# Performance work log

Hardware: AMD Instinct MI355X
Metric: run time of the kernel (lower is better)

The kernel has to match this reference:

```python
import jax, jax.numpy as jnp
import numpy as np

NUM_NODES = 100000
NUM_EDGES = 1600000
NUM_GRAPHS = 64
IN_DIM, HID, NCLS = 64, 128, 10


def setup_inputs() -> dict:
    key = jax.random.key(0)
    ks = jax.random.split(key, 12)
    x = jax.random.normal(ks[0], (NUM_NODES, IN_DIM), dtype=jnp.float32)
    src = jax.random.randint(ks[1], (NUM_EDGES,), 0, NUM_NODES, dtype=jnp.int32)
    dst = jax.random.randint(ks[2], (NUM_EDGES,), 0, NUM_NODES, dtype=jnp.int32)
    batch = jnp.sort(jax.random.randint(ks[3], (NUM_NODES,), 0, NUM_GRAPHS, dtype=jnp.int32))
    def glorot(k, shape):
        lim = (6.0 / (shape[0] + shape[1])) ** 0.5
        return jax.random.uniform(k, shape, jnp.float32, -lim, lim)
    return {
        "x": x, "src": src, "dst": dst, "batch": batch,
        "W1": glorot(ks[4], (IN_DIM, HID)), "b1": jnp.zeros((HID,), jnp.float32),
        "W2": glorot(ks[5], (HID, HID)), "b2": jnp.zeros((HID,), jnp.float32),
        "Wl1": glorot(ks[6], (HID, HID // 2)), "bl1": jnp.zeros((HID // 2,), jnp.float32),
        "Wl2": glorot(ks[7], (HID // 2, NCLS)), "bl2": jnp.zeros((NCLS,), jnp.float32),
    }


def gcn_conv(x, W, b, src, dst):
    # GCNConv: out = D^{-1/2} (A + I) D^{-1/2} (x @ W) + b, deg from A+I
    h = x @ W  # [N, H]
    ones = jnp.ones((src.shape[0],), h.dtype)
    deg = jax.ops.segment_sum(ones, dst, num_segments=NUM_NODES) + 1.0  # +1 self-loop
    dinv = jax.lax.rsqrt(deg)  # [N]
    norm = dinv[src] * dinv[dst]  # [E]
    msg = h[src] * norm[:, None]  # [E, H] gather + scale
    agg = jax.ops.segment_sum(msg, dst, num_segments=NUM_NODES)  # scatter-add
    agg = agg + h * (dinv * dinv)[:, None]  # self-loop message
    return agg + b


def reference(x, src, dst, batch, W1, b1, W2, b2, Wl1, bl1, Wl2, bl2):
    h = jax.nn.relu(gcn_conv(x, W1, b1, src, dst))
    h = jax.nn.relu(gcn_conv(h, W2, b2, src, dst))
    # global mean pool per graph
    sums = jax.ops.segment_sum(h, batch, num_segments=NUM_GRAPHS)  # [G, H]
    cnts = jax.ops.segment_sum(jnp.ones((h.shape[0],), h.dtype), batch, num_segments=NUM_GRAPHS)
    pooled = sums / jnp.maximum(cnts, 1.0)[:, None]
    h = jax.nn.relu(pooled @ Wl1 + bl1)
    return h @ Wl2 + bl2  # [G, num_classes]
```

## Files before the change

kernel.cpp:

```cpp
#include <hip/hip_runtime.h>
#include <hip/hip_bf16.h>

#define NODES_N 100000
#define EDGES_E 1600000
#define GRAPHS_G 64

#define BIN_SHIFT 8
#define BIN_NODES 256
#define NBINS 391
#define NB1 512
#define EPB1 3125

typedef unsigned int uint;
typedef unsigned short ushort;
typedef __attribute__((ext_vector_type(8))) short bf16x8;
typedef __attribute__((ext_vector_type(4))) float f32x4;


__device__ inline uint pack_bf2(float lo, float hi) {
    __hip_bfloat162 h2 = __float22bfloat162_rn(make_float2(lo, hi));
    return *reinterpret_cast<uint*>(&h2);
}

__device__ inline void acc_bf2(uint w, float& a0, float& a1) {
    a0 += __uint_as_float(w << 16);
    a1 += __uint_as_float(w & 0xffff0000u);
}

__device__ inline ushort f2bf(float v) {
    __hip_bfloat16 b = __float2bfloat16(v);
    return *reinterpret_cast<ushort*>(&b);
}


__device__ inline void pack_w_one(const float* W, ushort* Wf, int gid, int KS) {
    int j = gid & 7, l = (gid >> 3) & 63, f = gid >> 9;
    int nt = f / KS, ks = f - nt * KS;
    int k = ks * 32 + ((l >> 4) & 3) * 8 + j;
    int n = nt * 16 + (l & 15);
    Wf[gid] = f2bf(W[k * 128 + n]);
}

#define NZERO (GRAPHS_G * 128 + GRAPHS_G)

__global__ void pack_w_zero_k(const float* __restrict__ W1, ushort* __restrict__ W1f,
                              const float* __restrict__ W2, ushort* __restrict__ W2f,
                              float* __restrict__ zf) {
    int gid = blockIdx.x * 256 + threadIdx.x;
    if (gid < 8192) pack_w_one(W1, W1f, gid, 2);
    else if (gid < 24576) pack_w_one(W2, W2f, gid - 8192, 4);
    else {
        int i = gid - 24576;
        if (i < NZERO) zf[i] = 0.f;
    }
}


__global__ __launch_bounds__(256) void p1_hist_k(const int* __restrict__ dst,
                                                 int* __restrict__ hist_t) {
    __shared__ int h[NBINS];
    for (int i = threadIdx.x; i < NBINS; i += 256) h[i] = 0;
    __syncthreads();
    int b = blockIdx.x;
    int e0 = b * EPB1, e1 = min(EDGES_E, e0 + EPB1);
    for (int e = e0 + threadIdx.x; e < e1; e += 256)
        atomicAdd(&h[dst[e] >> BIN_SHIFT], 1);
    __syncthreads();
    for (int i = threadIdx.x; i < NBINS; i += 256)
        hist_t[i * NB1 + b] = h[i];
}

__global__ __launch_bounds__(256) void p1_scanbins_k(int* __restrict__ hist_t,
                                                     int* __restrict__ bintot) {
    __shared__ int sd[256];
    __shared__ int carry;
    int bin = blockIdx.x, t = threadIdx.x;
    if (t == 0) carry = 0;
    __syncthreads();
    int* row = hist_t + bin * NB1;
    for (int base = 0; base < NB1; base += 256) {
        int v = row[base + t];
        sd[t] = v; __syncthreads();
        for (int o = 1; o < 256; o <<= 1) {
            int x = (t >= o) ? sd[t - o] : 0;
            __syncthreads();
            sd[t] += x;
            __syncthreads();
        }
        row[base + t] = carry + sd[t] - v;
        __syncthreads();
        if (t == 255) carry += sd[255];
        __syncthreads();
    }
    if (t == 0) bintot[bin] = carry;
}

__global__ __launch_bounds__(1024) void binstart_k(const int* __restrict__ bintot,
                                                   int* __restrict__ binstart,
                                                   int* __restrict__ rowptr) {
    __shared__ int sd[1024];
    int t = threadIdx.x;
    int v = (t < NBINS) ? bintot[t] : 0;
    sd[t] = v; __syncthreads();
    for (int o = 1; o < 1024; o <<= 1) {
        int x = (t >= o) ? sd[t - o] : 0;
        __syncthreads();
        sd[t] += x;
        __syncthreads();
    }
    if (t < NBINS) binstart[t] = sd[t] - v;
    if (t == 0) { binstart[NBINS] = EDGES_E; rowptr[NODES_N] = EDGES_E; }
}

__global__ __launch_bounds__(256) void p1_scatter_k(const int* __restrict__ src,
                                                    const int* __restrict__ dst,
                                                    const int* __restrict__ hist_t,
                                                    const int* __restrict__ binstart,
                                                    uint* __restrict__ pairs) {
    __shared__ int cur[NBINS];
    int b = blockIdx.x;
    for (int i = threadIdx.x; i < NBINS; i += 256)
        cur[i] = binstart[i] + hist_t[i * NB1 + b];
    __syncthreads();
    int e0 = b * EPB1, e1 = min(EDGES_E, e0 + EPB1);
    for (int e = e0 + threadIdx.x; e < e1; e += 256) {
        int d = dst[e];
        int pos = atomicAdd(&cur[d >> BIN_SHIFT], 1);
        pairs[pos] = ((uint)src[e] << BIN_SHIFT) | (uint)(d & (BIN_NODES - 1));
    }
}

__global__ __launch_bounds__(256) void p2_build_k(const uint* __restrict__ pairs,
                                                  const int* __restrict__ binstart,
                                                  const float* __restrict__ x,
                                                  int* __restrict__ colidx,
                                                  int* __restrict__ rowptr,
                                                  float* __restrict__ dinv,
                                                  uint* __restrict__ xt) {
    __shared__ int h[BIN_NODES];
    __shared__ int off[BIN_NODES];
    __shared__ int cur[BIN_NODES];
    __shared__ float ldv[BIN_NODES];
    int bin = blockIdx.x, t = threadIdx.x;
    int node0 = bin << BIN_SHIFT;
    h[t] = 0;
    __syncthreads();
    int e0 = binstart[bin], e1 = binstart[bin + 1];
    for (int e = e0 + t; e < e1; e += 256)
        atomicAdd(&h[pairs[e] & (BIN_NODES - 1)], 1);
    __syncthreads();
    off[t] = h[t];
    __syncthreads();
    for (int o = 1; o < BIN_NODES; o <<= 1) {
        int x2 = (t >= o) ? off[t - o] : 0;
        __syncthreads();
        off[t] += x2;
        __syncthreads();
    }
    {
        int excl = off[t] - h[t];
        cur[t] = e0 + excl;
        float dv = rsqrtf((float)h[t] + 1.0f);
        ldv[t] = dv;
        int node = node0 + t;
        if (node < NODES_N) {
            rowptr[node] = e0 + excl;
            dinv[node] = dv;
        }
    }
    __syncthreads();
    for (int e = e0 + t; e < e1; e += 256) {
        uint p = pairs[e];
        int pos = atomicAdd(&cur[p & (BIN_NODES - 1)], 1);
        colidx[pos] = (int)(p >> BIN_SHIFT);
    }
    int nmax = min(NODES_N - node0, BIN_NODES);
    for (int i = t; i < nmax * 16; i += 256) {
        int nl = i >> 4, c = i & 15;
        int node = node0 + nl;
        float dv = ldv[nl];
        float4 v = *(const float4*)&x[(size_t)node * 64 + c * 4];
        uint2 o = make_uint2(pack_bf2(v.x * dv, v.y * dv), pack_bf2(v.z * dv, v.w * dv));
        *(uint2*)&xt[(size_t)node * 32 + c * 2] = o;
    }
}


__global__ __launch_bounds__(256) void gather64_k(const uint* __restrict__ xt,
                                                  const int* __restrict__ rowptr,
                                                  const int* __restrict__ colidx,
                                                  uint* __restrict__ st, int n) {
    int lane = threadIdx.x & 7;
    int local = threadIdx.x >> 3;
    int co = lane * 4;
    int node = blockIdx.x * 32 + local;
    if (node >= n) return;
    float a0=0,a1=0,a2=0,a3=0,a4=0,a5=0,a6=0,a7=0;
    uint4 v = *(const uint4*)&xt[(size_t)node * 32 + co];
    acc_bf2(v.x, a0, a1); acc_bf2(v.y, a2, a3);
    acc_bf2(v.z, a4, a5); acc_bf2(v.w, a6, a7);
    int beg = rowptr[node], end = rowptr[node + 1];
    int e = beg;
    for (; e + 7 < end; e += 8) {
        int i0 = colidx[e],   i1 = colidx[e+1], i2 = colidx[e+2], i3 = colidx[e+3];
        int i4 = colidx[e+4], i5 = colidx[e+5], i6 = colidx[e+6], i7 = colidx[e+7];
        uint4 w0 = *(const uint4*)&xt[(size_t)i0 * 32 + co];
        uint4 w1 = *(const uint4*)&xt[(size_t)i1 * 32 + co];
        uint4 w2 = *(const uint4*)&xt[(size_t)i2 * 32 + co];
        uint4 w3 = *(const uint4*)&xt[(size_t)i3 * 32 + co];
        uint4 w4 = *(const uint4*)&xt[(size_t)i4 * 32 + co];
        uint4 w5 = *(const uint4*)&xt[(size_t)i5 * 32 + co];
        uint4 w6 = *(const uint4*)&xt[(size_t)i6 * 32 + co];
        uint4 w7 = *(const uint4*)&xt[(size_t)i7 * 32 + co];
        acc_bf2(w0.x,a0,a1); acc_bf2(w0.y,a2,a3); acc_bf2(w0.z,a4,a5); acc_bf2(w0.w,a6,a7);
        acc_bf2(w1.x,a0,a1); acc_bf2(w1.y,a2,a3); acc_bf2(w1.z,a4,a5); acc_bf2(w1.w,a6,a7);
        acc_bf2(w2.x,a0,a1); acc_bf2(w2.y,a2,a3); acc_bf2(w2.z,a4,a5); acc_bf2(w2.w,a6,a7);
        acc_bf2(w3.x,a0,a1); acc_bf2(w3.y,a2,a3); acc_bf2(w3.z,a4,a5); acc_bf2(w3.w,a6,a7);
        acc_bf2(w4.x,a0,a1); acc_bf2(w4.y,a2,a3); acc_bf2(w4.z,a4,a5); acc_bf2(w4.w,a6,a7);
        acc_bf2(w5.x,a0,a1); acc_bf2(w5.y,a2,a3); acc_bf2(w5.z,a4,a5); acc_bf2(w5.w,a6,a7);
        acc_bf2(w6.x,a0,a1); acc_bf2(w6.y,a2,a3); acc_bf2(w6.z,a4,a5); acc_bf2(w6.w,a6,a7);
        acc_bf2(w7.x,a0,a1); acc_bf2(w7.y,a2,a3); acc_bf2(w7.z,a4,a5); acc_bf2(w7.w,a6,a7);
    }
    for (; e + 3 < end; e += 4) {
        int i0 = colidx[e], i1 = colidx[e+1], i2 = colidx[e+2], i3 = colidx[e+3];
        uint4 w0 = *(const uint4*)&xt[(size_t)i0 * 32 + co];
        uint4 w1 = *(const uint4*)&xt[(size_t)i1 * 32 + co];
        uint4 w2 = *(const uint4*)&xt[(size_t)i2 * 32 + co];
        uint4 w3 = *(const uint4*)&xt[(size_t)i3 * 32 + co];
        acc_bf2(w0.x,a0,a1); acc_bf2(w0.y,a2,a3); acc_bf2(w0.z,a4,a5); acc_bf2(w0.w,a6,a7);
        acc_bf2(w1.x,a0,a1); acc_bf2(w1.y,a2,a3); acc_bf2(w1.z,a4,a5); acc_bf2(w1.w,a6,a7);
        acc_bf2(w2.x,a0,a1); acc_bf2(w2.y,a2,a3); acc_bf2(w2.z,a4,a5); acc_bf2(w2.w,a6,a7);
        acc_bf2(w3.x,a0,a1); acc_bf2(w3.y,a2,a3); acc_bf2(w3.z,a4,a5); acc_bf2(w3.w,a6,a7);
    }
    for (; e < end; e++) {
        uint4 w0 = *(const uint4*)&xt[(size_t)colidx[e] * 32 + co];
        acc_bf2(w0.x,a0,a1); acc_bf2(w0.y,a2,a3); acc_bf2(w0.z,a4,a5); acc_bf2(w0.w,a6,a7);
    }
    uint4 o;
    o.x = pack_bf2(a0, a1);
    o.y = pack_bf2(a2, a3);
    o.z = pack_bf2(a4, a5);
    o.w = pack_bf2(a6, a7);
    *(uint4*)&st[(size_t)node * 32 + co] = o;
}


__global__ __launch_bounds__(256) void gemm_dual_k(const ushort* __restrict__ A,
                                                   const ushort* __restrict__ W1f,
                                                   const ushort* __restrict__ W2f,
                                                   const float* __restrict__ dinv,
                                                   const float* __restrict__ b1,
                                                   ushort* __restrict__ h2p, int n) {
    __shared__ ushort hl[4][16][132];
    int wave = threadIdx.x >> 6;
    int lane = threadIdx.x & 63;
    int row0 = (blockIdx.x * 4 + wave) * 16;
    if (row0 >= n) return;
    int m = lane & 15, g = lane >> 4;
    int arow = min(row0 + m, n - 1);

    const ushort* ab = &A[(size_t)arow * 64 + g * 8];
    bf16x8 a0 = *reinterpret_cast<const bf16x8*>(ab);
    bf16x8 a1 = *reinterpret_cast<const bf16x8*>(ab + 32);
    f32x4 acc[8];
#pragma unroll
    for (int nt = 0; nt < 8; nt++) {
        acc[nt] = (f32x4){0.f, 0.f, 0.f, 0.f};
        bf16x8 w0 = *reinterpret_cast<const bf16x8*>(&W1f[((size_t)(nt * 2 + 0) * 64 + lane) * 8]);
        bf16x8 w1 = *reinterpret_cast<const bf16x8*>(&W1f[((size_t)(nt * 2 + 1) * 64 + lane) * 8]);
        acc[nt] = __builtin_amdgcn_mfma_f32_16x16x32_bf16(a0, w0, acc[nt], 0, 0, 0);
        acc[nt] = __builtin_amdgcn_mfma_f32_16x16x32_bf16(a1, w1, acc[nt], 0, 0, 0);
    }

    int orow0 = row0 + g * 4;
#pragma unroll
    for (int r = 0; r < 4; r++) {
        float dvr = dinv[min(orow0 + r, n - 1)];
#pragma unroll
        for (int nt = 0; nt < 8; nt++) {
            float v = fmaxf(fmaf(dvr, acc[nt][r], b1[nt * 16 + m]), 0.f);
            hl[wave][g * 4 + r][nt * 16 + m] = f2bf(v);
        }
    }

    bf16x8 hfrag[4];
#pragma unroll
    for (int ks = 0; ks < 4; ks++) {
        uint2 lo = *(const uint2*)&hl[wave][m][g * 8 + ks * 32];
        uint2 hi = *(const uint2*)&hl[wave][m][g * 8 + ks * 32 + 4];
        uint4 u = make_uint4(lo.x, lo.y, hi.x, hi.y);
        hfrag[ks] = *reinterpret_cast<bf16x8*>(&u);
    }

    f32x4 acc2[8];
#pragma unroll
    for (int nt = 0; nt < 8; nt++) {
        acc2[nt] = (f32x4){0.f, 0.f, 0.f, 0.f};
#pragma unroll
        for (int ks = 0; ks < 4; ks++) {
            bf16x8 w = *reinterpret_cast<const bf16x8*>(&W2f[((size_t)(nt * 4 + ks) * 64 + lane) * 8]);
            acc2[nt] = __builtin_amdgcn_mfma_f32_16x16x32_bf16(hfrag[ks], w, acc2[nt], 0, 0, 0);
        }
    }

#pragma unroll
    for (int r = 0; r < 4; r++) {
        int row = orow0 + r;
        if (row < n) {
            float dvr = dinv[row];
#pragma unroll
            for (int nt = 0; nt < 8; nt++)
                h2p[(size_t)row * 128 + nt * 16 + m] = f2bf(acc2[nt][r] * dvr);
        }
    }
}


__global__ __launch_bounds__(256) void gather128_k(const uint* __restrict__ hp,
                                                   const int* __restrict__ rowptr,
                                                   const int* __restrict__ colidx,
                                                   const float* __restrict__ dinv,
                                                   const float* __restrict__ bias,
                                                   uint* __restrict__ h2b, int n) {
    int P = blockIdx.y;
    int lane = threadIdx.x & 7;
    int local = threadIdx.x >> 3;
    int co = P * 32 + lane * 4;
    int node = blockIdx.x * 32 + local;
    if (node >= n) return;
    float a0=0,a1=0,a2=0,a3=0,a4=0,a5=0,a6=0,a7=0;
    uint4 v = *(const uint4*)&hp[(size_t)node * 64 + co];
    acc_bf2(v.x, a0, a1); acc_bf2(v.y, a2, a3);
    acc_bf2(v.z, a4, a5); acc_bf2(v.w, a6, a7);
    int beg = rowptr[node], end = rowptr[node + 1];
    int e = beg;
    for (; e + 7 < end; e += 8) {
        int i0 = colidx[e],   i1 = colidx[e+1], i2 = colidx[e+2], i3 = colidx[e+3];
        int i4 = colidx[e+4], i5 = colidx[e+5], i6 = colidx[e+6], i7 = colidx[e+7];
        uint4 w0 = *(const uint4*)&hp[(size_t)i0 * 64 + co];
        uint4 w1 = *(const uint4*)&hp[(size_t)i1 * 64 + co];
        uint4 w2 = *(const uint4*)&hp[(size_t)i2 * 64 + co];
        uint4 w3 = *(const uint4*)&hp[(size_t)i3 * 64 + co];
        uint4 w4 = *(const uint4*)&hp[(size_t)i4 * 64 + co];
        uint4 w5 = *(const uint4*)&hp[(size_t)i5 * 64 + co];
        uint4 w6 = *(const uint4*)&hp[(size_t)i6 * 64 + co];
        uint4 w7 = *(const uint4*)&hp[(size_t)i7 * 64 + co];
        acc_bf2(w0.x,a0,a1); acc_bf2(w0.y,a2,a3); acc_bf2(w0.z,a4,a5); acc_bf2(w0.w,a6,a7);
        acc_bf2(w1.x,a0,a1); acc_bf2(w1.y,a2,a3); acc_bf2(w1.z,a4,a5); acc_bf2(w1.w,a6,a7);
        acc_bf2(w2.x,a0,a1); acc_bf2(w2.y,a2,a3); acc_bf2(w2.z,a4,a5); acc_bf2(w2.w,a6,a7);
        acc_bf2(w3.x,a0,a1); acc_bf2(w3.y,a2,a3); acc_bf2(w3.z,a4,a5); acc_bf2(w3.w,a6,a7);
        acc_bf2(w4.x,a0,a1); acc_bf2(w4.y,a2,a3); acc_bf2(w4.z,a4,a5); acc_bf2(w4.w,a6,a7);
        acc_bf2(w5.x,a0,a1); acc_bf2(w5.y,a2,a3); acc_bf2(w5.z,a4,a5); acc_bf2(w5.w,a6,a7);
        acc_bf2(w6.x,a0,a1); acc_bf2(w6.y,a2,a3); acc_bf2(w6.z,a4,a5); acc_bf2(w6.w,a6,a7);
        acc_bf2(w7.x,a0,a1); acc_bf2(w7.y,a2,a3); acc_bf2(w7.z,a4,a5); acc_bf2(w7.w,a6,a7);
    }
    for (; e + 3 < end; e += 4) {
        int i0 = colidx[e], i1 = colidx[e+1], i2 = colidx[e+2], i3 = colidx[e+3];
        uint4 w0 = *(const uint4*)&hp[(size_t)i0 * 64 + co];
        uint4 w1 = *(const uint4*)&hp[(size_t)i1 * 64 + co];
        uint4 w2 = *(const uint4*)&hp[(size_t)i2 * 64 + co];
        uint4 w3 = *(const uint4*)&hp[(size_t)i3 * 64 + co];
        acc_bf2(w0.x,a0,a1); acc_bf2(w0.y,a2,a3); acc_bf2(w0.z,a4,a5); acc_bf2(w0.w,a6,a7);
        acc_bf2(w1.x,a0,a1); acc_bf2(w1.y,a2,a3); acc_bf2(w1.z,a4,a5); acc_bf2(w1.w,a6,a7);
        acc_bf2(w2.x,a0,a1); acc_bf2(w2.y,a2,a3); acc_bf2(w2.z,a4,a5); acc_bf2(w2.w,a6,a7);
        acc_bf2(w3.x,a0,a1); acc_bf2(w3.y,a2,a3); acc_bf2(w3.z,a4,a5); acc_bf2(w3.w,a6,a7);
    }
    for (; e < end; e++) {
        uint4 w0 = *(const uint4*)&hp[(size_t)colidx[e] * 64 + co];
        acc_bf2(w0.x,a0,a1); acc_bf2(w0.y,a2,a3); acc_bf2(w0.z,a4,a5); acc_bf2(w0.w,a6,a7);
    }
    float dv = dinv[node];
    int jb = P * 64 + lane * 8;
    float4 b0 = *(const float4*)&bias[jb];
    float4 b1 = *(const float4*)&bias[jb + 4];
    float o0 = fmaxf(fmaf(dv, a0, b0.x), 0.f);
    float o1 = fmaxf(fmaf(dv, a1, b0.y), 0.f);
    float o2 = fmaxf(fmaf(dv, a2, b0.z), 0.f);
    float o3 = fmaxf(fmaf(dv, a3, b0.w), 0.f);
    float o4 = fmaxf(fmaf(dv, a4, b1.x), 0.f);
    float o5 = fmaxf(fmaf(dv, a5, b1.y), 0.f);
    float o6 = fmaxf(fmaf(dv, a6, b1.z), 0.f);
    float o7 = fmaxf(fmaf(dv, a7, b1.w), 0.f);
    uint4 ov;
    ov.x = pack_bf2(o0, o1);
    ov.y = pack_bf2(o2, o3);
    ov.z = pack_bf2(o4, o5);
    ov.w = pack_bf2(o6, o7);
    *(uint4*)&h2b[(size_t)node * 64 + co] = ov;
}


__global__ __launch_bounds__(128) void pool_k(const uint* __restrict__ h2b,
                                              const int* __restrict__ batch, int n,
                                              float* __restrict__ sums, float* __restrict__ cnts) {
    int j = threadIdx.x;
    int wj = j >> 1;
    int hi = j & 1;
    int chunk = (n + gridDim.x - 1) / gridDim.x;
    int i0 = blockIdx.x * chunk;
    int i1 = min(n, i0 + chunk);
    if (i0 >= n) return;
    int cur = batch[i0];
    float acc = 0.f;
    int cnt = 0;
    for (int i = i0; i < i1; i++) {
        int g = batch[i];
        if (g != cur) {
            atomicAdd(&sums[cur * 128 + j], acc);
            if (j == 0) atomicAdd(&cnts[cur], (float)cnt);
            acc = 0.f; cnt = 0; cur = g;
        }
        uint w = h2b[(size_t)i * 64 + wj];
        acc += __uint_as_float(hi ? (w & 0xffff0000u) : (w << 16));
        cnt++;
    }
    atomicAdd(&sums[cur * 128 + j], acc);
    if (j == 0) atomicAdd(&cnts[cur], (float)cnt);
}


__global__ __launch_bounds__(64) void mlp_k(const float* __restrict__ sums, const float* __restrict__ cnts,
                                            const float* __restrict__ Wl1, const float* __restrict__ bl1,
                                            const float* __restrict__ Wl2, const float* __restrict__ bl2,
                                            float* __restrict__ out) {
    __shared__ float pooled[128];
    __shared__ float hidden[64];
    int g = blockIdx.x, t = threadIdx.x;
    float c = fmaxf(cnts[g], 1.0f);
    pooled[t]      = sums[g * 128 + t] / c;
    pooled[t + 64] = sums[g * 128 + 64 + t] / c;
    __syncthreads();
    float a = bl1[t];
#pragma unroll 4
    for (int cc = 0; cc < 128; cc++) a = fmaf(pooled[cc], Wl1[cc * 64 + t], a);
    hidden[t] = fmaxf(a, 0.f);
    __syncthreads();
    if (t < 10) {
        float o = bl2[t];
#pragma unroll 8
        for (int jj = 0; jj < 64; jj++) o = fmaf(hidden[jj], Wl2[jj * 10 + t], o);
        out[g * 10 + t] = o;
    }
}


extern "C" void kernel_launch(void* const* d_in, const int* in_sizes, int n_in,
                              void* d_out, int out_size, void* d_ws, size_t ws_size,
                              hipStream_t stream) {
    const float* x    = (const float*)d_in[0];
    const int*   src  = (const int*)d_in[1];
    const int*   dst  = (const int*)d_in[2];
    const int*   batch= (const int*)d_in[3];
    const float* W1   = (const float*)d_in[4];
    const float* b1   = (const float*)d_in[5];
    const float* W2   = (const float*)d_in[6];
    const float* b2   = (const float*)d_in[7];
    const float* Wl1  = (const float*)d_in[8];
    const float* bl1  = (const float*)d_in[9];
    const float* Wl2  = (const float*)d_in[10];
    const float* bl2  = (const float*)d_in[11];
    float* out = (float*)d_out;

    const int N = NODES_N;

    size_t off = 0;
    auto take = [&](size_t bytes) { size_t o = off; off = (off + bytes + 255) & ~(size_t)255; return o; };
    char* ws = (char*)d_ws;
    uint*   h2p  = (uint*)(ws + take((size_t)N * 128 * 2));
    uint*   h2b  = (uint*)(ws + take((size_t)N * 128 * 2));
    size_t  shbytes = (size_t)N * 64 * 2;
    char*   shreg = ws + take(shbytes);
    uint*   pairs = (uint*)shreg;
    uint*   stil  = (uint*)shreg;
    uint*   xt   = (uint*)(ws + take((size_t)N * 64 * 2));
    float*  dinv = (float*)(ws + take((size_t)N * 4));
    ushort* W1f  = (ushort*)(ws + take((size_t)64 * 128 * 2));
    ushort* W2f  = (ushort*)(ws + take((size_t)128 * 128 * 2));
    size_t zbytes = (size_t)NZERO * 4;
    char*  zbase  = ws + take(zbytes);
    float* sums   = (float*)zbase;
    float* cnts   = (float*)(zbase + (size_t)GRAPHS_G * 128 * 4);
    int*   rowptr = (int*)(ws + take((size_t)(N + 1) * 4));
    int*   colidx = (int*)(ws + take((size_t)EDGES_E * 4));
    int*   hist_t = (int*)(ws + take((size_t)NBINS * NB1 * 4));
    int*   bintot = (int*)(ws + take((size_t)NBINS * 4));
    int*   binstart = (int*)(ws + take((size_t)(NBINS + 1) * 4));
    (void)ws_size; (void)in_sizes; (void)n_in; (void)out_size;

    pack_w_zero_k<<<(24576 + NZERO + 255) / 256, 256, 0, stream>>>(W1, W1f, W2, W2f, sums);

    p1_hist_k<<<NB1, 256, 0, stream>>>(dst, hist_t);
    p1_scanbins_k<<<NBINS, 256, 0, stream>>>(hist_t, bintot);
    binstart_k<<<1, 1024, 0, stream>>>(bintot, binstart, rowptr);
    p1_scatter_k<<<NB1, 256, 0, stream>>>(src, dst, hist_t, binstart, pairs);
    p2_build_k<<<NBINS, 256, 0, stream>>>(pairs, binstart, x, colidx, rowptr, dinv, xt);

    int g32 = (N + 31) / 32;
    gather64_k<<<g32, 256, 0, stream>>>(xt, rowptr, colidx, stil, N);

    int gblk = (N + 63) / 64;
    gemm_dual_k<<<gblk, 256, 0, stream>>>((const ushort*)stil, W1f, W2f, dinv, b1, (ushort*)h2p, N);

    gather128_k<<<dim3(g32, 2), 256, 0, stream>>>(h2p, rowptr, colidx, dinv, b2, h2b, N);

    pool_k<<<1024, 128, 0, stream>>>(h2b, batch, N, sums, cnts);
    mlp_k<<<GRAPHS_G, 64, 0, stream>>>(sums, cnts, Wl1, bl1, Wl2, bl2, out);
}
```

Baseline: 212.0 us.

## Reorder gather nodes by in-degree bucket to balance wavefront work

Builds a per-degree histogram in p2_build_k and a new perm_k kernel that counting-sorts nodes by in-degree (capped at 63) into a permutation. Both gather kernels then process nodes in that order, so the 8-lane groups within a wavefront see similar edge counts and spend fewer cycles idle on divergence. In exchange it adds a kernel launch, global atomics, and an extra indirection. Output rows become scattered rather than contiguous, which may weaken write coalescing and locality.

```diff
diff --git a/kernel.cpp b/kernel.cpp
--- a/kernel.cpp
+++ b/kernel.cpp
@@ -41,7 +41,7 @@
     Wf[gid] = f2bf(W[k * 128 + n]);
 }
 
-#define NZERO (GRAPHS_G * 128 + GRAPHS_G)
+#define NZERO (GRAPHS_G * 128 + GRAPHS_G + 128)
 
 __global__ void pack_w_zero_k(const float* __restrict__ W1, ushort* __restrict__ W1f,
                               const float* __restrict__ W2, ushort* __restrict__ W2f,
@@ -136,14 +136,17 @@
                                                   int* __restrict__ colidx,
                                                   int* __restrict__ rowptr,
                                                   float* __restrict__ dinv,
-                                                  uint* __restrict__ xt) {
+                                                  uint* __restrict__ xt,
+                                                  int* __restrict__ dhist) {
     __shared__ int h[BIN_NODES];
     __shared__ int off[BIN_NODES];
     __shared__ int cur[BIN_NODES];
     __shared__ float ldv[BIN_NODES];
+    __shared__ int dgh[64];
     int bin = blockIdx.x, t = threadIdx.x;
     int node0 = bin << BIN_SHIFT;
     h[t] = 0;
+    if (t < 64) dgh[t] = 0;
     __syncthreads();
     int e0 = binstart[bin], e1 = binstart[bin + 1];
     for (int e = e0 + t; e < e1; e += 256)
@@ -166,6 +169,7 @@
         if (node < NODES_N) {
             rowptr[node] = e0 + excl;
             dinv[node] = dv;
+            atomicAdd(&dgh[min(h[t], 63)], 1);
         }
     }
     __syncthreads();
@@ -183,18 +187,59 @@
         uint2 o = make_uint2(pack_bf2(v.x * dv, v.y * dv), pack_bf2(v.z * dv, v.w * dv));
         *(uint2*)&xt[(size_t)node * 32 + c * 2] = o;
     }
+    __syncthreads();
+    if (t < 64 && dgh[t] > 0) atomicAdd(&dhist[t], dgh[t]);
+}
+
+
+__global__ __launch_bounds__(256) void perm_k(const int* __restrict__ rowptr,
+                                              const int* __restrict__ dhist,
+                                              int* __restrict__ dcur,
+                                              int* __restrict__ perm) {
+    __shared__ int dh[64], dstart[64], dbase[64], dloc[64];
+    int b = blockIdx.x, t = threadIdx.x;
+    if (t < 64) { dh[t] = 0; dloc[t] = 0; }
+    __syncthreads();
+    int node = (b << BIN_SHIFT) + t;
+    bool act = node < NODES_N;
+    int bk = 0;
+    if (act) {
+        int deg = rowptr[node + 1] - rowptr[node];
+        bk = min(deg, 63);
+        atomicAdd(&dh[bk], 1);
+    }
+    __syncthreads();
+    if (t < 64) dstart[t] = dhist[t];
+    __syncthreads();
+    for (int o = 1; o < 64; o <<= 1) {
+        int x = (t >= o && t < 64) ? dstart[t - o] : 0;
+        __syncthreads();
+        if (t < 64) dstart[t] += x;
+        __syncthreads();
+    }
+    if (t < 64) {
+        int excl = dstart[t] - dhist[t];
+        dbase[t] = (dh[t] > 0) ? excl + atomicAdd(&dcur[t], dh[t]) : 0;
+    }
+    __syncthreads();
+    if (act) {
+        int r = atomicAdd(&dloc[bk], 1);
+        perm[dbase[bk] + r] = node;
+    }
 }
 
 
 __global__ __launch_bounds__(256) void gather64_k(const uint* __restrict__ xt,
                                                   const int* __restrict__ rowptr,
                                                   const int* __restrict__ colidx,
+                                                  const int* __restrict__ perm,
                                                   uint* __restrict__ st, int n) {
     int lane = threadIdx.x & 7;
     int local = threadIdx.x >> 3;
     int co = lane * 4;
-    int node = blockIdx.x * 32 + local;
-    if (node >= n) return;
+    int idx = blockIdx.x * 32 + local;
+    if (idx >= n) return;
+    int node = perm[idx];
     float a0=0,a1=0,a2=0,a3=0,a4=0,a5=0,a6=0,a7=0;
     uint4 v = *(const uint4*)&xt[(size_t)node * 32 + co];
     acc_bf2(v.x, a0, a1); acc_bf2(v.y, a2, a3);
@@ -319,6 +364,7 @@
 __global__ __launch_bounds__(256) void gather128_k(const uint* __restrict__ hp,
                                                    const int* __restrict__ rowptr,
                                                    const int* __restrict__ colidx,
+                                                   const int* __restrict__ perm,
                                                    const float* __restrict__ dinv,
                                                    const float* __restrict__ bias,
                                                    uint* __restrict__ h2b, int n) {
@@ -326,8 +372,9 @@
     int lane = threadIdx.x & 7;
     int local = threadIdx.x >> 3;
     int co = P * 32 + lane * 4;
-    int node = blockIdx.x * 32 + local;
-    if (node >= n) return;
+    int idx = blockIdx.x * 32 + local;
+    if (idx >= n) return;
+    int node = perm[idx];
     float a0=0,a1=0,a2=0,a3=0,a4=0,a5=0,a6=0,a7=0;
     uint4 v = *(const uint4*)&hp[(size_t)node * 64 + co];
     acc_bf2(v.x, a0, a1); acc_bf2(v.y, a2, a3);
@@ -480,8 +527,11 @@
     char*  zbase  = ws + take(zbytes);
     float* sums   = (float*)zbase;
     float* cnts   = (float*)(zbase + (size_t)GRAPHS_G * 128 * 4);
+    int*   dhist  = (int*)(zbase + (size_t)(GRAPHS_G * 128 + GRAPHS_G) * 4);
+    int*   dcur   = dhist + 64;
     int*   rowptr = (int*)(ws + take((size_t)(N + 1) * 4));
     int*   colidx = (int*)(ws + take((size_t)EDGES_E * 4));
+    int*   perm   = (int*)(ws + take((size_t)N * 4));
     int*   hist_t = (int*)(ws + take((size_t)NBINS * NB1 * 4));
     int*   bintot = (int*)(ws + take((size_t)NBINS * 4));
     int*   binstart = (int*)(ws + take((size_t)(NBINS + 1) * 4));
@@ -493,15 +543,17 @@
     p1_scanbins_k<<<NBINS, 256, 0, stream>>>(hist_t, bintot);
     binstart_k<<<1, 1024, 0, stream>>>(bintot, binstart, rowptr);
     p1_scatter_k<<<NB1, 256, 0, stream>>>(src, dst, hist_t, binstart, pairs);
-    p2_build_k<<<NBINS, 256, 0, stream>>>(pairs, binstart, x, colidx, rowptr, dinv, xt);
+    p2_build_k<<<NBINS, 256, 0, stream>>>(pairs, binstart, x, colidx, rowptr, dinv, xt, dhist);
+
+    perm_k<<<NBINS, 256, 0, stream>>>(rowptr, dhist, dcur, perm);
 
     int g32 = (N + 31) / 32;
-    gather64_k<<<g32, 256, 0, stream>>>(xt, rowptr, colidx, stil, N);
+    gather64_k<<<g32, 256, 0, stream>>>(xt, rowptr, colidx, perm, stil, N);
 
     int gblk = (N + 63) / 64;
     gemm_dual_k<<<gblk, 256, 0, stream>>>((const ushort*)stil, W1f, W2f, dinv, b1, (ushort*)h2p, N);
 
-    gather128_k<<<dim3(g32, 2), 256, 0, stream>>>(h2p, rowptr, colidx, dinv, b2, h2b, N);
+    gather128_k<<<dim3(g32, 2), 256, 0, stream>>>(h2p, rowptr, colidx, perm, dinv, b2, h2b, N);
 
     pool_k<<<1024, 128, 0, stream>>>(h2b, batch, N, sums, cnts);
     mlp_k<<<GRAPHS_G, 64, 0, stream>>>(sums, cnts, Wl1, bl1, Wl2, bl2, out);
```

After: 225.0 us. 6.1% more time.
